# Kernel optimization log

Hardware: AMD Instinct MI355X
Metric: run time of the kernel (lower is better)

## Reference

```python
import jax, jax.numpy as jnp
import numpy as np

B, S, D, H = 4, 2048, 1024, 16
DK = D // H

def setup_inputs() -> dict:
    key = jax.random.key(0)
    ks = jax.random.split(key, 11)
    scale = 1.0 / np.sqrt(D)
    return {
        "query": jax.random.normal(ks[0], (B, S, D), jnp.float32),
        "key_": jax.random.normal(ks[1], (B, S, D), jnp.float32),
        "value": jax.random.normal(ks[2], (B, S, D), jnp.float32),
        "Wq": jax.random.normal(ks[3], (D, D), jnp.float32) * scale,
        "bq": jnp.zeros((D,), jnp.float32),
        "Wk": jax.random.normal(ks[4], (D, D), jnp.float32) * scale,
        "bk": jnp.zeros((D,), jnp.float32),
        "Wv": jax.random.normal(ks[5], (D, D), jnp.float32) * scale,
        "bv": jnp.zeros((D,), jnp.float32),
        "Wo": jax.random.normal(ks[6], (D, D), jnp.float32) * scale,
        "bo": jnp.zeros((D,), jnp.float32),
    }

def reference(query, key_, value, Wq, bq, Wk, bk, Wv, bv, Wo, bo):
    # Linear projections (torch Linear: x @ W.T + b)
    Q = query @ Wq.T + bq            # [B,S,D]
    K = key_ @ Wk.T + bk
    V = value @ Wv.T + bv
    # split heads -> [B,H,S,DK]
    def split(x):
        return x.reshape(B, S, H, DK).transpose(0, 2, 1, 3)
    Qh, Kh, Vh = split(Q), split(K), split(V)
    scores = jnp.einsum("bhqd,bhkd->bhqk", Qh, Kh) / np.sqrt(DK)
    attn = jax.nn.softmax(scores, axis=-1)
    ctx = jnp.einsum("bhqk,bhkd->bhqd", attn, Vh)
    ctx = ctx.transpose(0, 2, 1, 3).reshape(B, S, D)
    return ctx @ Wo.T + bo
```

## Files before the change

kernel.cpp:

```cpp
#include <hip/hip_runtime.h>
#include <hip/hip_bf16.h>
#include <stdint.h>

#define B_ 4
#define S_ 2048
#define D_ 1024
#define H_ 16
#define DK_ 64
#define GM (B_ * S_)
#define GN D_
#define GK D_
#define BM 128
#define BN 128
#define BK 64
#define QBLK 128

typedef __attribute__((ext_vector_type(8))) __bf16 bf16x8;
typedef __attribute__((ext_vector_type(4))) float f32x4;
typedef __attribute__((ext_vector_type(4))) uint32_t u32x4;

#if __has_builtin(__builtin_amdgcn_exp2f)
#define EXP2F(x) __builtin_amdgcn_exp2f(x)
#else
#define EXP2F(x) exp2f(x)
#endif

__device__ __forceinline__ uint16_t f2bf(float x) {
  uint32_t u = __builtin_bit_cast(uint32_t, x);
  u += 0x7fffu + ((u >> 16) & 1u);
  return (uint16_t)(u >> 16);
}
__device__ __forceinline__ void gload_lds16(const void* g, void* l) {
  __builtin_amdgcn_global_load_lds(
      (const __attribute__((address_space(1))) void*)g,
      (__attribute__((address_space(3))) void*)l, 16, 0, 0);
}

__device__ __forceinline__ int swzK(int kv, int colb) {
  return colb ^ ((kv & 7) << 4);
}
__device__ __forceinline__ int swzV(int dk, int off) {
  return off ^ ((((dk >> 3) ^ dk) & 7) << 4);
}
__device__ __forceinline__ int swzP(int q, int off) {
  return off ^ ((q & 7) << 4) ^ (((q >> 2) & 3) << 5);
}

struct CvtArgs {
  const float* src[7];
  uint16_t* dst[7];
  int n[7];
};

__global__ __launch_bounds__(256) void cvt_f32_bf16(CvtArgs a) {
  const int z = blockIdx.z;
  const float* __restrict__ s = a.src[z];
  uint16_t* __restrict__ d = a.dst[z];
  const int nv = a.n[z] >> 3;
  const int stride = gridDim.x * blockDim.x;
  for (int i = blockIdx.x * blockDim.x + threadIdx.x; i < nv; i += stride) {
    f32x4 v0 = *(const f32x4*)(s + (size_t)i * 8);
    f32x4 v1 = *(const f32x4*)(s + (size_t)i * 8 + 4);
    union { uint16_t u[8]; u32x4 q; } o;
#pragma unroll
    for (int j = 0; j < 4; ++j) o.u[j] = f2bf(v0[j]);
#pragma unroll
    for (int j = 0; j < 4; ++j) o.u[4 + j] = f2bf(v1[j]);
    *(u32x4*)(d + (size_t)i * 8) = o.q;
  }
}

struct Gemm3Args {
  const uint16_t* A[3];
  const uint16_t* W[3];
  const float* bias[3];
  void* C[3];
};

template <bool CF32>
__global__ __launch_bounds__(256, 2) void mha_gemm3(Gemm3Args args) {
  const int z = blockIdx.z;
  const char* __restrict__ A = (const char*)args.A[z];
  const char* __restrict__ W = (const char*)args.W[z];
  const float* __restrict__ bias = args.bias[z];
  void* __restrict__ C = args.C[z];

  __shared__ alignas(16) uint16_t tA[BM][BK];
  __shared__ alignas(16) uint16_t tW[BN][BK];

  const int tid = threadIdx.x;
  const int lane = tid & 63;
  const int wid = tid >> 6;
  const int wm = wid >> 1, wn = wid & 1;
  const int l16 = lane & 15, g = lane >> 4;

  const int m0 = blockIdx.y * BM;
  const int n0 = blockIdx.x * BN;

  f32x4 acc[4][4] = {};
  const int o = tid * 16;

  for (int k0 = 0; k0 < GK; k0 += BK) {
#pragma unroll
    for (int i = 0; i < 4; ++i) {
      const int oo = o + i * 4096;
      const int row = oo >> 7, colb = oo & 127;
      gload_lds16(A + (size_t)(m0 + row) * (GK * 2) + (size_t)k0 * 2 + colb,
                  ((char*)&tA[0][0]) + i * 4096 + wid * 1024);
      gload_lds16(W + (size_t)(n0 + row) * (GK * 2) + (size_t)k0 * 2 + colb,
                  ((char*)&tW[0][0]) + i * 4096 + wid * 1024);
    }
    __syncthreads();
#pragma unroll
    for (int kk = 0; kk < 2; ++kk) {
      const int kcol = kk * 32 + g * 8;
      bf16x8 af[4], bfr[4];
#pragma unroll
      for (int m = 0; m < 4; ++m)
        af[m] = *(const bf16x8*)&tA[wm * 64 + m * 16 + l16][kcol];
#pragma unroll
      for (int n = 0; n < 4; ++n)
        bfr[n] = *(const bf16x8*)&tW[wn * 64 + n * 16 + l16][kcol];
#pragma unroll
      for (int m = 0; m < 4; ++m)
#pragma unroll
        for (int n = 0; n < 4; ++n)
          acc[m][n] = __builtin_amdgcn_mfma_f32_16x16x32_bf16(
              af[m], bfr[n], acc[m][n], 0, 0, 0);
    }
    __syncthreads();
  }

#pragma unroll
  for (int n = 0; n < 4; ++n) {
    const int col = n0 + wn * 64 + n * 16 + l16;
    const float bv = bias[col];
#pragma unroll
    for (int m = 0; m < 4; ++m) {
      const int rbase = m0 + wm * 64 + m * 16 + g * 4;
#pragma unroll
      for (int r = 0; r < 4; ++r) {
        const float v = acc[m][n][r] + bv;
        if (CF32)
          ((float*)C)[(size_t)(rbase + r) * GN + col] = v;
        else
          ((uint16_t*)C)[(size_t)(rbase + r) * GN + col] = f2bf(v);
      }
    }
  }
}

__global__ __launch_bounds__(256) void mha_attn(
    const uint16_t* __restrict__ Q, const uint16_t* __restrict__ K,
    const uint16_t* __restrict__ V, uint16_t* __restrict__ O) {
  __shared__ alignas(16) char K_s[64 * 128];
  __shared__ alignas(16) char V_s[64 * 128];
  __shared__ alignas(16) char P_s[4 * 32 * 128];

  const int tid = threadIdx.x;
  const int lane = tid & 63;
  const int wid = tid >> 6;
  const int l16 = lane & 15, g = lane >> 4;
  const int bh = blockIdx.y;
  const int b = bh >> 4, h = bh & 15;
  const int q0 = blockIdx.x * QBLK;

  bf16x8 qf[2][2];
#pragma unroll
  for (int mi = 0; mi < 2; ++mi) {
    const uint16_t* qp = Q + ((size_t)(b * S_) + q0 + mi * 64 + wid * 16 + l16) * D_ +
                         h * DK_ + g * 8;
    qf[mi][0] = *(const bf16x8*)qp;
    qf[mi][1] = *(const bf16x8*)(qp + 32);
  }

  f32x4 o_acc[2][4] = {};
  float lpart[2][4] = {};
  const float sc = 0.18033688011112042f;

  const char* Kb = (const char*)K;
  const char* Vb = (const char*)V;
  const size_t rowb = (size_t)D_ * 2;
  const size_t headoff = (size_t)h * DK_ * 2;
  char* P_w = P_s + wid * 4096;

  for (int kv0 = 0; kv0 < S_; kv0 += 64) {
#pragma unroll
    for (int i = 0; i < 2; ++i) {
      const int oo = tid * 16 + i * 4096;
      const int row = oo >> 7, colb = oo & 127;
      const size_t gro = ((size_t)(b * S_) + kv0 + row) * rowb + headoff + colb;
      u32x4 kk_ = *(const u32x4*)(Kb + gro);
      *(u32x4*)(K_s + row * 128 + swzK(row, colb)) = kk_;
      u32x4 vv = *(const u32x4*)(Vb + gro);
      const int c0 = colb >> 1;
#pragma unroll
      for (int j = 0; j < 4; ++j) {
        const uint32_t w = vv[j];
        const int dk0 = c0 + 2 * j, dk1 = dk0 + 1;
        *(uint16_t*)(V_s + dk0 * 128 + swzV(dk0, row * 2)) = (uint16_t)(w & 0xffffu);
        *(uint16_t*)(V_s + dk1 * 128 + swzV(dk1, row * 2)) = (uint16_t)(w >> 16);
      }
    }
    __syncthreads();

    f32x4 sacc[2][4] = {};
#pragma unroll
    for (int ks = 0; ks < 2; ++ks) {
      const int kcolb = ks * 64 + g * 16;
#pragma unroll
      for (int n = 0; n < 4; ++n) {
        const int kvr = n * 16 + l16;
        const bf16x8 kf = *(const bf16x8*)(K_s + kvr * 128 + swzK(kvr, kcolb));
#pragma unroll
        for (int mi = 0; mi < 2; ++mi)
          sacc[mi][n] = __builtin_amdgcn_mfma_f32_16x16x32_bf16(
              qf[mi][ks], kf, sacc[mi][n], 0, 0, 0);
      }
    }

#pragma unroll
    for (int mi = 0; mi < 2; ++mi)
#pragma unroll
      for (int n = 0; n < 4; ++n)
#pragma unroll
        for (int r = 0; r < 4; ++r) {
          const float p = EXP2F(sacc[mi][n][r] * sc);
          lpart[mi][r] += p;
          const int q = mi * 16 + g * 4 + r;
          const int off = (n * 16 + l16) * 2;
          *(uint16_t*)(P_w + q * 128 + swzP(q, off)) = f2bf(p);
        }

#pragma unroll
    for (int ks = 0; ks < 2; ++ks) {
      const int kcolb = ks * 64 + g * 16;
      bf16x8 pf[2];
#pragma unroll
      for (int mi = 0; mi < 2; ++mi) {
        const int q = mi * 16 + l16;
        pf[mi] = *(const bf16x8*)(P_w + q * 128 + swzP(q, kcolb));
      }
#pragma unroll
      for (int n = 0; n < 4; ++n) {
        const int dk = n * 16 + l16;
        const bf16x8 vf = *(const bf16x8*)(V_s + dk * 128 + swzV(dk, kcolb));
#pragma unroll
        for (int mi = 0; mi < 2; ++mi)
          o_acc[mi][n] = __builtin_amdgcn_mfma_f32_16x16x32_bf16(
              pf[mi], vf, o_acc[mi][n], 0, 0, 0);
      }
    }
    __syncthreads();
  }

  float linv[2][4];
#pragma unroll
  for (int mi = 0; mi < 2; ++mi)
#pragma unroll
    for (int r = 0; r < 4; ++r) {
      float s_ = lpart[mi][r];
#pragma unroll
      for (int msk = 1; msk < 16; msk <<= 1) s_ += __shfl_xor(s_, msk, 64);
      linv[mi][r] = 1.f / s_;
    }

#pragma unroll
  for (int mi = 0; mi < 2; ++mi) {
    const int qrow = q0 + mi * 64 + wid * 16 + g * 4;
#pragma unroll
    for (int n = 0; n < 4; ++n) {
      const int col = h * DK_ + n * 16 + l16;
#pragma unroll
      for (int r = 0; r < 4; ++r) {
        const float v = o_acc[mi][n][r] * linv[mi][r];
        O[((size_t)(b * S_) + qrow + r) * D_ + col] = f2bf(v);
      }
    }
  }
}

extern "C" void kernel_launch(void* const* d_in, const int* in_sizes, int n_in,
                              void* d_out, int out_size, void* d_ws,
                              size_t ws_size, hipStream_t stream) {
  (void)in_sizes; (void)n_in; (void)out_size; (void)ws_size;

  const float* query = (const float*)d_in[0];
  const float* key_ = (const float*)d_in[1];
  const float* value = (const float*)d_in[2];
  const float* Wq = (const float*)d_in[3];
  const float* bq = (const float*)d_in[4];
  const float* Wk = (const float*)d_in[5];
  const float* bk = (const float*)d_in[6];
  const float* Wv = (const float*)d_in[7];
  const float* bv = (const float*)d_in[8];
  const float* Wo = (const float*)d_in[9];
  const float* bo = (const float*)d_in[10];

  const size_t nact = (size_t)GM * GN;
  const size_t nw = (size_t)GN * GK;
  uint16_t* p = (uint16_t*)d_ws;
  uint16_t* qb = p; p += nact;
  uint16_t* kb = p; p += nact;
  uint16_t* vb = p; p += nact;
  uint16_t* wq = p; p += nw;
  uint16_t* wk = p; p += nw;
  uint16_t* wv = p; p += nw;
  uint16_t* wo = p; p += nw;
  uint16_t* Qp = p; p += nact;
  uint16_t* Kp = p; p += nact;
  uint16_t* Vp = p; p += nact;
  uint16_t* Cp = p; p += nact;

  CvtArgs ca;
  const float* srcs[7] = {query, key_, value, Wq, Wk, Wv, Wo};
  uint16_t* dsts[7] = {qb, kb, vb, wq, wk, wv, wo};
  const int cnts[7] = {(int)nact, (int)nact, (int)nact, (int)nw,
                       (int)nw,   (int)nw,   (int)nw};
  for (int i = 0; i < 7; ++i) {
    ca.src[i] = srcs[i]; ca.dst[i] = dsts[i]; ca.n[i] = cnts[i];
  }
  cvt_f32_bf16<<<dim3(512, 1, 7), dim3(256), 0, stream>>>(ca);

  Gemm3Args g1;
  g1.A[0] = qb; g1.A[1] = kb; g1.A[2] = vb;
  g1.W[0] = wq; g1.W[1] = wk; g1.W[2] = wv;
  g1.bias[0] = bq; g1.bias[1] = bk; g1.bias[2] = bv;
  g1.C[0] = Qp; g1.C[1] = Kp; g1.C[2] = Vp;
  mha_gemm3<false>
      <<<dim3(GN / BN, GM / BM, 3), dim3(256), 0, stream>>>(g1);

  mha_attn<<<dim3(S_ / QBLK, B_ * H_), dim3(256), 0, stream>>>(Qp, Kp, Vp, Cp);

  Gemm3Args g2;
  g2.A[0] = Cp; g2.W[0] = wo; g2.bias[0] = bo; g2.C[0] = d_out;
  g2.A[1] = g2.A[0]; g2.W[1] = g2.W[0]; g2.bias[1] = g2.bias[0]; g2.C[1] = g2.C[0];
  g2.A[2] = g2.A[0]; g2.W[2] = g2.W[0]; g2.bias[2] = g2.bias[0]; g2.C[2] = g2.C[0];
  mha_gemm3<true>
      <<<dim3(GN / BN, GM / BM, 1), dim3(256), 0, stream>>>(g2);
}
```

Baseline: 276.7 us.

## Double-buffer K/V tiles in attention and fold softmax scale into Wq

The attention kernel now keeps two K/V shared-memory buffers. The next tile's K is issued as an asynchronous global-to-LDS load and its V is prefetched into registers while the current tile is being computed, then V is transposed into the other buffer after the PV step. This drops one barrier per iteration and overlaps global latency with MFMA work. The 1/sqrt(dk)*log2e scale is folded into the bf16 conversion of Wq and into the Q bias, which removes a per-element multiply before exp2 but rounds the scaled weights to bf16 and doubles K/V LDS use.

```diff
diff --git a/kernel.cpp b/kernel.cpp
--- a/kernel.cpp
+++ b/kernel.cpp
@@ -25,6 +25,8 @@
 #define EXP2F(x) exp2f(x)
 #endif
 
+#define SCALE_LOG2E 0.18033688011112042f
+
 __device__ __forceinline__ uint16_t f2bf(float x) {
   uint32_t u = __builtin_bit_cast(uint32_t, x);
   u += 0x7fffu + ((u >> 16) & 1u);
@@ -50,12 +52,14 @@
   const float* src[7];
   uint16_t* dst[7];
   int n[7];
+  float scale[7];
 };
 
 __global__ __launch_bounds__(256) void cvt_f32_bf16(CvtArgs a) {
   const int z = blockIdx.z;
   const float* __restrict__ s = a.src[z];
   uint16_t* __restrict__ d = a.dst[z];
+  const float sc = a.scale[z];
   const int nv = a.n[z] >> 3;
   const int stride = gridDim.x * blockDim.x;
   for (int i = blockIdx.x * blockDim.x + threadIdx.x; i < nv; i += stride) {
@@ -63,9 +67,9 @@
     f32x4 v1 = *(const f32x4*)(s + (size_t)i * 8 + 4);
     union { uint16_t u[8]; u32x4 q; } o;
 #pragma unroll
-    for (int j = 0; j < 4; ++j) o.u[j] = f2bf(v0[j]);
-#pragma unroll
-    for (int j = 0; j < 4; ++j) o.u[4 + j] = f2bf(v1[j]);
+    for (int j = 0; j < 4; ++j) o.u[j] = f2bf(v0[j] * sc);
+#pragma unroll
+    for (int j = 0; j < 4; ++j) o.u[4 + j] = f2bf(v1[j] * sc);
     *(u32x4*)(d + (size_t)i * 8) = o.q;
   }
 }
@@ -74,6 +78,7 @@
   const uint16_t* A[3];
   const uint16_t* W[3];
   const float* bias[3];
+  float bscale[3];
   void* C[3];
 };
 
@@ -83,6 +88,7 @@
   const char* __restrict__ A = (const char*)args.A[z];
   const char* __restrict__ W = (const char*)args.W[z];
   const float* __restrict__ bias = args.bias[z];
+  const float bsc = args.bscale[z];
   void* __restrict__ C = args.C[z];
 
   __shared__ alignas(16) uint16_t tA[BM][BK];
@@ -134,7 +140,7 @@
 #pragma unroll
   for (int n = 0; n < 4; ++n) {
     const int col = n0 + wn * 64 + n * 16 + l16;
-    const float bv = bias[col];
+    const float bv = bias[col] * bsc;
 #pragma unroll
     for (int m = 0; m < 4; ++m) {
       const int rbase = m0 + wm * 64 + m * 16 + g * 4;
@@ -153,8 +159,8 @@
 __global__ __launch_bounds__(256) void mha_attn(
     const uint16_t* __restrict__ Q, const uint16_t* __restrict__ K,
     const uint16_t* __restrict__ V, uint16_t* __restrict__ O) {
-  __shared__ alignas(16) char K_s[64 * 128];
-  __shared__ alignas(16) char V_s[64 * 128];
+  __shared__ alignas(16) char K_s[2][64 * 128];
+  __shared__ alignas(16) char V_s[2][64 * 128];
   __shared__ alignas(16) char P_s[4 * 32 * 128];
 
   const int tid = threadIdx.x;
@@ -176,7 +182,6 @@
 
   f32x4 o_acc[2][4] = {};
   float lpart[2][4] = {};
-  const float sc = 0.18033688011112042f;
 
   const char* Kb = (const char*)K;
   const char* Vb = (const char*)V;
@@ -184,25 +189,48 @@
   const size_t headoff = (size_t)h * DK_ * 2;
   char* P_w = P_s + wid * 4096;
 
+  int srow[2], scolb[2];
+#pragma unroll
+  for (int i = 0; i < 2; ++i) {
+    const int oo = tid * 16 + i * 4096;
+    srow[i] = oo >> 7;
+    scolb[i] = oo & 127;
+  }
+
+#define ISSUE_LOADS(buf, kv0, vreg)                                            \
+  {                                                                            \
+    _Pragma("unroll") for (int i = 0; i < 2; ++i) {                            \
+      const size_t base = ((size_t)(b * S_) + (kv0) + srow[i]) * rowb + headoff;\
+      gload_lds16(Kb + base + (scolb[i] ^ ((srow[i] & 7) << 4)),               \
+                  &K_s[buf][0] + i * 4096 + wid * 1024);                       \
+      vreg[i] = *(const u32x4*)(Vb + base + scolb[i]);                         \
+    }                                                                          \
+  }
+
+#define WRITE_V(buf, vreg)                                                     \
+  {                                                                            \
+    _Pragma("unroll") for (int i = 0; i < 2; ++i) {                            \
+      const int c0 = scolb[i] >> 1;                                            \
+      _Pragma("unroll") for (int j = 0; j < 4; ++j) {                          \
+        const uint32_t w = vreg[i][j];                                         \
+        const int dk0 = c0 + 2 * j, dk1 = dk0 + 1;                             \
+        *(uint16_t*)(&V_s[buf][0] + dk0 * 128 + swzV(dk0, srow[i] * 2)) =      \
+            (uint16_t)(w & 0xffffu);                                           \
+        *(uint16_t*)(&V_s[buf][0] + dk1 * 128 + swzV(dk1, srow[i] * 2)) =      \
+            (uint16_t)(w >> 16);                                               \
+      }                                                                        \
+    }                                                                          \
+  }
+
+  u32x4 vreg[2];
+  ISSUE_LOADS(0, 0, vreg);
+  WRITE_V(0, vreg);
+  __syncthreads();
+  int cur = 0;
+
   for (int kv0 = 0; kv0 < S_; kv0 += 64) {
-#pragma unroll
-    for (int i = 0; i < 2; ++i) {
-      const int oo = tid * 16 + i * 4096;
-      const int row = oo >> 7, colb = oo & 127;
-      const size_t gro = ((size_t)(b * S_) + kv0 + row) * rowb + headoff + colb;
-      u32x4 kk_ = *(const u32x4*)(Kb + gro);
-      *(u32x4*)(K_s + row * 128 + swzK(row, colb)) = kk_;
-      u32x4 vv = *(const u32x4*)(Vb + gro);
-      const int c0 = colb >> 1;
-#pragma unroll
-      for (int j = 0; j < 4; ++j) {
-        const uint32_t w = vv[j];
-        const int dk0 = c0 + 2 * j, dk1 = dk0 + 1;
-        *(uint16_t*)(V_s + dk0 * 128 + swzV(dk0, row * 2)) = (uint16_t)(w & 0xffffu);
-        *(uint16_t*)(V_s + dk1 * 128 + swzV(dk1, row * 2)) = (uint16_t)(w >> 16);
-      }
-    }
-    __syncthreads();
+    const bool last = (kv0 + 64 >= S_);
+    if (!last) ISSUE_LOADS(cur ^ 1, kv0 + 64, vreg);
 
     f32x4 sacc[2][4] = {};
 #pragma unroll
@@ -211,7 +239,8 @@
 #pragma unroll
       for (int n = 0; n < 4; ++n) {
         const int kvr = n * 16 + l16;
-        const bf16x8 kf = *(const bf16x8*)(K_s + kvr * 128 + swzK(kvr, kcolb));
+        const bf16x8 kf =
+            *(const bf16x8*)(&K_s[cur][0] + kvr * 128 + swzK(kvr, kcolb));
 #pragma unroll
         for (int mi = 0; mi < 2; ++mi)
           sacc[mi][n] = __builtin_amdgcn_mfma_f32_16x16x32_bf16(
@@ -225,7 +254,7 @@
       for (int n = 0; n < 4; ++n)
 #pragma unroll
         for (int r = 0; r < 4; ++r) {
-          const float p = EXP2F(sacc[mi][n][r] * sc);
+          const float p = EXP2F(sacc[mi][n][r]);
           lpart[mi][r] += p;
           const int q = mi * 16 + g * 4 + r;
           const int off = (n * 16 + l16) * 2;
@@ -244,14 +273,20 @@
 #pragma unroll
       for (int n = 0; n < 4; ++n) {
         const int dk = n * 16 + l16;
-        const bf16x8 vf = *(const bf16x8*)(V_s + dk * 128 + swzV(dk, kcolb));
+        const bf16x8 vf =
+            *(const bf16x8*)(&V_s[cur][0] + dk * 128 + swzV(dk, kcolb));
 #pragma unroll
         for (int mi = 0; mi < 2; ++mi)
           o_acc[mi][n] = __builtin_amdgcn_mfma_f32_16x16x32_bf16(
               pf[mi], vf, o_acc[mi][n], 0, 0, 0);
       }
     }
-    __syncthreads();
+
+    if (!last) {
+      WRITE_V(cur ^ 1, vreg);
+      __syncthreads();
+    }
+    cur ^= 1;
   }
 
   float linv[2][4];
@@ -319,13 +354,16 @@
                        (int)nw,   (int)nw,   (int)nw};
   for (int i = 0; i < 7; ++i) {
     ca.src[i] = srcs[i]; ca.dst[i] = dsts[i]; ca.n[i] = cnts[i];
-  }
+    ca.scale[i] = 1.0f;
+  }
+  ca.scale[3] = SCALE_LOG2E;
   cvt_f32_bf16<<<dim3(512, 1, 7), dim3(256), 0, stream>>>(ca);
 
   Gemm3Args g1;
   g1.A[0] = qb; g1.A[1] = kb; g1.A[2] = vb;
   g1.W[0] = wq; g1.W[1] = wk; g1.W[2] = wv;
   g1.bias[0] = bq; g1.bias[1] = bk; g1.bias[2] = bv;
+  g1.bscale[0] = SCALE_LOG2E; g1.bscale[1] = 1.0f; g1.bscale[2] = 1.0f;
   g1.C[0] = Qp; g1.C[1] = Kp; g1.C[2] = Vp;
   mha_gemm3<false>
       <<<dim3(GN / BN, GM / BM, 3), dim3(256), 0, stream>>>(g1);
@@ -334,8 +372,11 @@
 
   Gemm3Args g2;
   g2.A[0] = Cp; g2.W[0] = wo; g2.bias[0] = bo; g2.C[0] = d_out;
+  g2.bscale[0] = 1.0f;
   g2.A[1] = g2.A[0]; g2.W[1] = g2.W[0]; g2.bias[1] = g2.bias[0]; g2.C[1] = g2.C[0];
+  g2.bscale[1] = 1.0f;
   g2.A[2] = g2.A[0]; g2.W[2] = g2.W[0]; g2.bias[2] = g2.bias[0]; g2.C[2] = g2.C[0];
+  g2.bscale[2] = 1.0f;
   mha_gemm3<true>
       <<<dim3(GN / BN, GM / BM, 1), dim3(256), 0, stream>>>(g2);
 }
```

New measurement: 264.9 us. 1.04x faster.
